# Optimization experiments

Measured on AMD Instinct MI355X. Metric: run time of the kernel, lower is better.

The kernel has to match this reference:

```python
import jax, jax.numpy as jnp
import numpy as np

DEPTH = 5
EPS = 1e-8


def setup_inputs() -> dict:
    key = jax.random.key(0)
    ks = jax.random.split(key, 7)
    N, E, Q = 50000, 1600000, 16
    return {
        "marg_i": jax.random.normal(ks[0], (N, Q), dtype=jnp.float32),
        "cav_ij": jax.random.uniform(ks[1], (E, Q), dtype=jnp.float32),
        "C": jax.random.uniform(ks[2], (Q, Q), dtype=jnp.float32),
        "field_i": jax.random.normal(ks[3], (N, Q), dtype=jnp.float32),
        "edge_dst": jax.random.randint(ks[4], (E,), 0, N, dtype=jnp.int32),
        "a1_src": jax.random.randint(ks[5], (E,), 0, N, dtype=jnp.int32),
        "indice_ij": jax.random.randint(ks[6], (E,), 0, E, dtype=jnp.int32),
    }


def reference(marg_i, cav_ij, C, field_i, edge_dst, a1_src, indice_ij):
    # Belief-propagation layers repeated DEPTH times.
    # B_ @ temp2  -> segment_sum of edge messages into destination nodes [N,Q]
    # A1 @ marg_i -> gather of source-node marginal per edge [E,Q]
    N = field_i.shape[0]

    def step(carry, _):
        marg, cav = carry
        temp2 = jnp.log(cav @ C + EPS)                                  # [E,Q]
        marg = jax.ops.segment_sum(temp2, edge_dst, num_segments=N) + field_i  # [N,Q]
        cav = jax.nn.softmax(marg[a1_src] - temp2[indice_ij], axis=1)  # [E,Q]
        return (marg, cav), None

    (marg, cav), _ = jax.lax.scan(step, (marg_i, cav_ij), None, length=DEPTH)
    return jax.nn.log_softmax(marg, axis=1)
```

## Files before the change

### kernel.cpp

```cpp
#include <hip/hip_runtime.h>
#include <hip/hip_fp16.h>

#define Q 16
#define EPS 1e-8f
#define DEPTH 5
#define BS 512
#define WSHIFT 9

typedef unsigned int u32;
typedef _Float16 h2 __attribute__((ext_vector_type(2)));

typedef int   i2v __attribute__((ext_vector_type(2)));
typedef u32   u4v __attribute__((ext_vector_type(4)));
typedef float f4v __attribute__((ext_vector_type(4)));

__device__ __forceinline__ int nt_ld(const int* p) {
    return __builtin_nontemporal_load(p);
}
__device__ __forceinline__ void nt_st(int* p, int v) {
    __builtin_nontemporal_store(v, p);
}
__device__ __forceinline__ int2 nt_ld2(const int2* p) {
    i2v r = __builtin_nontemporal_load((const i2v*)p);
    return make_int2(r.x, r.y);
}
__device__ __forceinline__ void nt_st2(int2* p, int2 v) {
    i2v t; t.x = v.x; t.y = v.y;
    __builtin_nontemporal_store(t, (i2v*)p);
}
__device__ __forceinline__ float4 nt_ldf4(const float4* p) {
    f4v r = __builtin_nontemporal_load((const f4v*)p);
    return make_float4(r.x, r.y, r.z, r.w);
}
__device__ __forceinline__ void nt_stf4(float4* p, float4 v) {
    f4v t; t.x = v.x; t.y = v.y; t.z = v.z; t.w = v.w;
    __builtin_nontemporal_store(t, (f4v*)p);
}
__device__ __forceinline__ void nt_stu4(uint4* p, uint4 v) {
    u4v t; t.x = v.x; t.y = v.y; t.z = v.z; t.w = v.w;
    __builtin_nontemporal_store(t, (u4v*)p);
}

__device__ __forceinline__ u32 pack2(float a, float b) {
    __half2 h = __floats2half2_rn(a, b);
    return *(u32*)&h;
}
__device__ __forceinline__ float2 unpack2(u32 u) {
    __half2 h = *(__half2*)&u;
    return __half22float2(h);
}
__device__ __forceinline__ h2 mkh2(float a, float b) {
    h2 v; v[0] = (_Float16)a; v[1] = (_Float16)b; return v;
}


__global__ __launch_bounds__(256) void rank0_kernel(
    const int* __restrict__ dst, int* __restrict__ count,
    int* __restrict__ lr, int E)
{
    int e = blockIdx.x * 256 + threadIdx.x;
    if (e < E) nt_st(&lr[e], atomicAdd(&count[nt_ld(&dst[e])], 1));
}

__global__ __launch_bounds__(256) void scan_partial(
    const int* __restrict__ count, int* __restrict__ partial, int N)
{
    __shared__ int sm[256];
    int i = blockIdx.x * 256 + threadIdx.x;
    sm[threadIdx.x] = (i < N) ? count[i] : 0;
    __syncthreads();
    for (int off = 128; off > 0; off >>= 1) {
        if (threadIdx.x < off) sm[threadIdx.x] += sm[threadIdx.x + off];
        __syncthreads();
    }
    if (threadIdx.x == 0) partial[blockIdx.x] = sm[0];
}

__global__ __launch_bounds__(1024) void scan_top(
    int* __restrict__ partial, int nb)
{
    __shared__ int sm[1024];
    int t = threadIdx.x;
    int v = (t < nb) ? partial[t] : 0;
    sm[t] = v;
    __syncthreads();
    for (int off = 1; off < 1024; off <<= 1) {
        int u = (t >= off) ? sm[t - off] : 0;
        __syncthreads();
        sm[t] += u;
        __syncthreads();
    }
    if (t < nb) partial[t] = sm[t] - v;
}

__global__ __launch_bounds__(256) void scan_final(
    const int* __restrict__ count, const int* __restrict__ partial,
    int* __restrict__ start, int N)
{
    __shared__ int sm[256];
    int i = blockIdx.x * 256 + threadIdx.x;
    int v = (i < N) ? count[i] : 0;
    sm[threadIdx.x] = v;
    __syncthreads();
    for (int off = 1; off < 256; off <<= 1) {
        int u = (threadIdx.x >= off) ? sm[threadIdx.x - off] : 0;
        __syncthreads();
        sm[threadIdx.x] += u;
        __syncthreads();
    }
    int excl = sm[threadIdx.x] - v + partial[blockIdx.x];
    if (i < N) start[i] = excl;
    if (i == N - 1) start[N] = excl + v;
}

__global__ __launch_bounds__(256) void pos_kernel(
    const int* __restrict__ dst, const int* __restrict__ lr,
    const int* __restrict__ start, int* __restrict__ pos, int E)
{
    int e = blockIdx.x * 256 + threadIdx.x;
    if (e < E) pos[e] = start[nt_ld(&dst[e])] + nt_ld(&lr[e]);
}

__global__ __launch_bounds__(256) void scatter_direct(
    const int* __restrict__ a1_src, const int* __restrict__ indice,
    const int* __restrict__ dst, const int* __restrict__ pos,
    int2* __restrict__ meta2, int* __restrict__ m0e, int E)
{
    int e = blockIdx.x * 256 + threadIdx.x;
    if (e < E) {
        int p = nt_ld(&pos[e]);
        int ie = nt_ld(&indice[e]);
        int2 mv = make_int2(pos[ie],
                            (int)(((u32)nt_ld(&dst[e]) << 16) | (u32)nt_ld(&a1_src[e])));
        nt_st2(&meta2[p], mv);
        nt_st(&m0e[p], e);
    }
}

__global__ __launch_bounds__(256) void bnode_build(
    const int* __restrict__ start, int* __restrict__ blist,
    int* __restrict__ bcount, int N)
{
    int n = blockIdx.x * 256 + threadIdx.x;
    if (n >= N) return;
    int slo = start[n], shi = start[n + 1];
    bool need = (slo == shi) || ((slo >> WSHIFT) != ((shi - 1) >> WSHIFT));
    if (need) {
        int p = atomicAdd(bcount, 1);
        blist[p] = n;
    }
}

__global__ __launch_bounds__(256) void binit(
    const int* __restrict__ blist, const int* __restrict__ bcount,
    const float* __restrict__ field, float* __restrict__ marg)
{
    int idx = blockIdx.x * 256 + threadIdx.x;
    int cnt = *bcount;
    if (idx >= cnt * 4) return;
    int n = blist[idx >> 2], part = idx & 3;
    ((float4*)(marg + (size_t)n * Q))[part] =
        ((const float4*)(field + (size_t)n * Q))[part];
}

template<int MODE>
__global__ __launch_bounds__(BS) void fused_round(
    const int2* __restrict__ meta2, const int* __restrict__ m0e,
    const float* __restrict__ C,
    const float* __restrict__ cav,
    const float* __restrict__ marg_in, const u32* __restrict__ t2_old,
    const int* __restrict__ start, const float* __restrict__ field,
    u32* __restrict__ t2_new, float* __restrict__ marg_out, int E)
{
    __shared__ __align__(16) h2 Csh[Q * 8];
    __shared__ float stage[BS * 17];
    __shared__ int s_nfirst, s_nlast;

    const int tid = threadIdx.x;
    const int blo = blockIdx.x * BS;
    const int bhi = min(blo + BS, E);
    const int j = blo + tid;
    const bool act = (j < E);

    int2 meta;
    float4 m0, m1, m2, m3;
    uint4 r0, r1;
    if (act) {
        meta = nt_ld2(&meta2[j]);
        if (MODE == 0) {
            const float4* rp = (const float4*)(cav + (size_t)nt_ld(&m0e[j]) * Q);
            m0 = nt_ldf4(rp + 0); m1 = nt_ldf4(rp + 1);
            m2 = nt_ldf4(rp + 2); m3 = nt_ldf4(rp + 3);
        } else {
            const int src = meta.y & 0xffff;
            const float4* mp = (const float4*)(marg_in + (size_t)src * Q);
            const uint4*  tp = (const uint4*)(t2_old + (size_t)meta.x * 8);
            m0 = mp[0]; m1 = mp[1]; m2 = mp[2]; m3 = mp[3];
            r0 = tp[0]; r1 = tp[1];
        }
    }

    if (tid < 128) {
        int q = tid >> 3, kk = tid & 7;
        Csh[q * 8 + kk] = mkh2(C[(2 * kk) * Q + q], C[(2 * kk + 1) * Q + q]);
    }
    if (act) {
        int mydst = (int)(((u32)meta.y) >> 16);
        if (j == blo)     s_nfirst = mydst;
        if (j == bhi - 1) s_nlast  = mydst;
    }
    __syncthreads();

    float t[Q];
    if (act) {
        h2 uh[8];
        float s, logs;
        if (MODE == 0) {
            uh[0] = mkh2(m0.x, m0.y); uh[1] = mkh2(m0.z, m0.w);
            uh[2] = mkh2(m1.x, m1.y); uh[3] = mkh2(m1.z, m1.w);
            uh[4] = mkh2(m2.x, m2.y); uh[5] = mkh2(m2.z, m2.w);
            uh[6] = mkh2(m3.x, m3.y); uh[7] = mkh2(m3.z, m3.w);
            s = 1.f; logs = 0.f;
        } else {
            float2 p0 = unpack2(r0.x), p1 = unpack2(r0.y),
                   p2 = unpack2(r0.z), p3 = unpack2(r0.w);
            float2 p4 = unpack2(r1.x), p5 = unpack2(r1.y),
                   p6 = unpack2(r1.z), p7 = unpack2(r1.w);

            float x[Q] = {m0.x - p0.x, m0.y - p0.y, m0.z - p1.x, m0.w - p1.y,
                          m1.x - p2.x, m1.y - p2.y, m1.z - p3.x, m1.w - p3.y,
                          m2.x - p4.x, m2.y - p4.y, m2.z - p5.x, m2.w - p5.y,
                          m3.x - p6.x, m3.y - p6.y, m3.z - p7.x, m3.w - p7.y};

            float mx = x[0];
#pragma unroll
            for (int q = 1; q < Q; ++q) mx = fmaxf(mx, x[q]);
            float u[Q];
            s = 0.f;
#pragma unroll
            for (int q = 0; q < Q; ++q) { u[q] = __expf(x[q] - mx); s += u[q]; }
            logs = __logf(s);
#pragma unroll
            for (int k = 0; k < 8; ++k) uh[k] = mkh2(u[2 * k], u[2 * k + 1]);
        }

        const float base = EPS * s;
#pragma unroll
        for (int q = 0; q < Q; ++q) {
            const uint4* cp = (const uint4*)&Csh[q * 8];
            h2 col[8];
            ((uint4*)col)[0] = cp[0];
            ((uint4*)col)[1] = cp[1];
            float acc = base;
#pragma unroll
            for (int kk = 0; kk < 8; ++kk)
                acc = __builtin_amdgcn_fdot2(uh[kk], col[kk], acc, false);
            t[q] = __logf(acc) - logs;
        }

        if (MODE != 2) {
            uint4 w0, w1;
            w0.x = pack2(t[0],  t[1]);  w0.y = pack2(t[2],  t[3]);
            w0.z = pack2(t[4],  t[5]);  w0.w = pack2(t[6],  t[7]);
            w1.x = pack2(t[8],  t[9]);  w1.y = pack2(t[10], t[11]);
            w1.z = pack2(t[12], t[13]); w1.w = pack2(t[14], t[15]);
            uint4* op = (uint4*)(t2_new + (size_t)j * 8);
            nt_stu4(op + 0, w0);
            nt_stu4(op + 1, w1);
        }
    } else {
#pragma unroll
        for (int q = 0; q < Q; ++q) t[q] = 0.f;
    }

#pragma unroll
    for (int q = 0; q < Q; ++q) stage[tid * 17 + q] = t[q];
    __syncthreads();

    const int nfirst = s_nfirst;
    const int ncnt = s_nlast - nfirst + 1;
    for (int k = tid; k < ncnt * Q; k += BS) {
        int ln = k >> 4, q = k & 15;
        int n = nfirst + ln;
        int slo = start[n], shi = start[n + 1];
        int lo = max(slo, blo), hi = min(shi, bhi);
        float s = 0.f;
        for (int sl = lo; sl < hi; ++sl) s += stage[(sl - blo) * 17 + q];
        if (slo >= blo && shi <= bhi)
            marg_out[(size_t)n * Q + q] = s + field[(size_t)n * Q + q];
        else
            atomicAdd(marg_out + (size_t)n * Q + q, s);
    }
}

__global__ __launch_bounds__(256) void node_out(
    const float* __restrict__ marg, float* __restrict__ out, int N)
{
    int i = blockIdx.x * 256 + threadIdx.x;
    if (i >= N) return;

    const float4* mp = (const float4*)(marg + (size_t)i * Q);
    float4 m0 = nt_ldf4(mp + 0), m1 = nt_ldf4(mp + 1),
           m2 = nt_ldf4(mp + 2), m3 = nt_ldf4(mp + 3);
    float x[Q] = {m0.x, m0.y, m0.z, m0.w, m1.x, m1.y, m1.z, m1.w,
                  m2.x, m2.y, m2.z, m2.w, m3.x, m3.y, m3.z, m3.w};

    float mx = x[0];
#pragma unroll
    for (int q = 1; q < Q; ++q) mx = fmaxf(mx, x[q]);
    float s = 0.f;
#pragma unroll
    for (int q = 0; q < Q; ++q) s += __expf(x[q] - mx);
    float lse = mx + __logf(s);

    float4* op = (float4*)(out + (size_t)i * Q);
    nt_stf4(op + 0, make_float4(x[0]  - lse, x[1]  - lse, x[2]  - lse, x[3]  - lse));
    nt_stf4(op + 1, make_float4(x[4]  - lse, x[5]  - lse, x[6]  - lse, x[7]  - lse));
    nt_stf4(op + 2, make_float4(x[8]  - lse, x[9]  - lse, x[10] - lse, x[11] - lse));
    nt_stf4(op + 3, make_float4(x[12] - lse, x[13] - lse, x[14] - lse, x[15] - lse));
}

extern "C" void kernel_launch(void* const* d_in, const int* in_sizes, int n_in,
                              void* d_out, int out_size, void* d_ws, size_t ws_size,
                              hipStream_t stream) {
    const float* cav_in   = (const float*)d_in[1];
    const float* C        = (const float*)d_in[2];
    const float* field_i  = (const float*)d_in[3];
    const int*   edge_dst = (const int*)d_in[4];
    const int*   a1_src   = (const int*)d_in[5];
    const int*   indice   = (const int*)d_in[6];
    float* out = (float*)d_out;

    const int E = in_sizes[4];
    const int N = in_sizes[0] / Q;

    char* ws = (char*)d_ws;
    const size_t t2_bytes   = (size_t)E * 32;
    const size_t node_bytes = (size_t)N * Q * sizeof(float);
    u32*   t2a    = (u32*)ws;                     ws += t2_bytes;
    u32*   t2b    = (u32*)ws;                     ws += t2_bytes;
    int2*  meta2  = (int2*)ws;                    ws += (size_t)E * 8;
    int*   m0e    = (int*)ws;                     ws += (size_t)E * 4;
    float* marg_a = (float*)ws;                   ws += node_bytes;
    float* marg_b = (float*)ws;                   ws += node_bytes;
    int*   pos    = (int*)ws;                     ws += (size_t)E * 4;
    int*   lr     = (int*)ws;                     ws += (size_t)E * 4;
    int*   count  = (int*)ws;                     ws += (size_t)N * 4;
    int*   bcount = (int*)ws;                     ws += 4;
    int*   start  = (int*)ws;                     ws += (size_t)(N + 1) * 4;
    int*   blist  = (int*)ws;                     ws += (size_t)N * 4;
    int*   partial= (int*)ws;

    const int eb = 256;
    const int eg = (E + eb - 1) / eb;
    const int fg = (E + BS - 1) / BS;
    const int ng = (N + eb - 1) / eb;

    hipMemsetAsync(count, 0, (size_t)N * 4 + 4, stream);
    rank0_kernel<<<eg, eb, 0, stream>>>(edge_dst, count, lr, E);
    scan_partial<<<ng, eb, 0, stream>>>(count, partial, N);
    scan_top<<<1, 1024, 0, stream>>>(partial, ng);
    scan_final<<<ng, eb, 0, stream>>>(count, partial, start, N);
    pos_kernel<<<eg, eb, 0, stream>>>(edge_dst, lr, start, pos, E);
    scatter_direct<<<eg, eb, 0, stream>>>(a1_src, indice, edge_dst, pos,
                                          meta2, m0e, E);
    bnode_build<<<ng, eb, 0, stream>>>(start, blist, bcount, N);

    u32* t_cur = t2a;
    u32* t_nxt = t2b;
    float* m_in = marg_b;
    float* m_out = marg_a;
    const int bg = (N * 4 + eb - 1) / eb;

    for (int it = 0; it < DEPTH; ++it) {
        binit<<<bg, eb, 0, stream>>>(blist, bcount, field_i, m_out);
        if (it == 0)
            fused_round<0><<<fg, BS, 0, stream>>>(meta2, m0e, C, cav_in,
                                                  nullptr, nullptr, start, field_i,
                                                  t_cur, m_out, E);
        else if (it != DEPTH - 1)
            fused_round<1><<<fg, BS, 0, stream>>>(meta2, m0e, C, nullptr,
                                                  m_in, t_cur, start, field_i,
                                                  t_nxt, m_out, E);
        else
            fused_round<2><<<fg, BS, 0, stream>>>(meta2, m0e, C, nullptr,
                                                  m_in, t_cur, start, field_i,
                                                  nullptr, m_out, E);
        if (it != 0) { u32* tt = t_cur; t_cur = t_nxt; t_nxt = tt; }
        float* tm = m_in; m_in = m_out; m_out = tm;
    }

    node_out<<<ng, eb, 0, stream>>>(m_in, out, N);
}
```

Measured before the change: 712.2 us.

## Fuse preprocessing kernels and pack sorted edge metadata into int4

Packs each edge's destination and local rank into one word so the separate position kernel can be dropped, and folds boundary-node detection into the final scan kernel. Scatter now computes sorted positions on the fly and writes one 16-byte record holding the reverse-edge position, dst/src and original edge id, replacing the separate meta2 and m0e arrays. Nontemporal hints on the metadata load and the t2 stores are removed, so those accesses may now stay in cache. The trade-off is 16 bytes of metadata per edge read in every round instead of 8 (plus 4 in the first round), and a packed format that caps the per-node rank at 16 bits.

```diff
diff --git a/kernel.cpp b/kernel.cpp
--- a/kernel.cpp
+++ b/kernel.cpp
@@ -10,23 +10,10 @@
 typedef unsigned int u32;
 typedef _Float16 h2 __attribute__((ext_vector_type(2)));
 
-typedef int   i2v __attribute__((ext_vector_type(2)));
-typedef u32   u4v __attribute__((ext_vector_type(4)));
 typedef float f4v __attribute__((ext_vector_type(4)));
 
 __device__ __forceinline__ int nt_ld(const int* p) {
     return __builtin_nontemporal_load(p);
-}
-__device__ __forceinline__ void nt_st(int* p, int v) {
-    __builtin_nontemporal_store(v, p);
-}
-__device__ __forceinline__ int2 nt_ld2(const int2* p) {
-    i2v r = __builtin_nontemporal_load((const i2v*)p);
-    return make_int2(r.x, r.y);
-}
-__device__ __forceinline__ void nt_st2(int2* p, int2 v) {
-    i2v t; t.x = v.x; t.y = v.y;
-    __builtin_nontemporal_store(t, (i2v*)p);
 }
 __device__ __forceinline__ float4 nt_ldf4(const float4* p) {
     f4v r = __builtin_nontemporal_load((const f4v*)p);
@@ -36,10 +23,6 @@
     f4v t; t.x = v.x; t.y = v.y; t.z = v.z; t.w = v.w;
     __builtin_nontemporal_store(t, (f4v*)p);
 }
-__device__ __forceinline__ void nt_stu4(uint4* p, uint4 v) {
-    u4v t; t.x = v.x; t.y = v.y; t.z = v.z; t.w = v.w;
-    __builtin_nontemporal_store(t, (u4v*)p);
-}
 
 __device__ __forceinline__ u32 pack2(float a, float b) {
     __half2 h = __floats2half2_rn(a, b);
@@ -56,10 +39,14 @@
 
 __global__ __launch_bounds__(256) void rank0_kernel(
     const int* __restrict__ dst, int* __restrict__ count,
-    int* __restrict__ lr, int E)
+    int* __restrict__ lrd, int E)
 {
     int e = blockIdx.x * 256 + threadIdx.x;
-    if (e < E) nt_st(&lr[e], atomicAdd(&count[nt_ld(&dst[e])], 1));
+    if (e < E) {
+        int d = nt_ld(&dst[e]);
+        int r = atomicAdd(&count[d], 1);
+        lrd[e] = (int)(((u32)d << 16) | (u32)r);
+    }
 }
 
 __global__ __launch_bounds__(256) void scan_partial(
@@ -95,7 +82,8 @@
 
 __global__ __launch_bounds__(256) void scan_final(
     const int* __restrict__ count, const int* __restrict__ partial,
-    int* __restrict__ start, int N)
+    int* __restrict__ start, int* __restrict__ blist,
+    int* __restrict__ bcount, int N)
 {
     __shared__ int sm[256];
     int i = blockIdx.x * 256 + threadIdx.x;
@@ -109,45 +97,31 @@
         __syncthreads();
     }
     int excl = sm[threadIdx.x] - v + partial[blockIdx.x];
-    if (i < N) start[i] = excl;
+    if (i < N) {
+        start[i] = excl;
+        bool need = (v == 0) || ((excl >> WSHIFT) != ((excl + v - 1) >> WSHIFT));
+        if (need) {
+            int p = atomicAdd(bcount, 1);
+            blist[p] = i;
+        }
+    }
     if (i == N - 1) start[N] = excl + v;
 }
 
-__global__ __launch_bounds__(256) void pos_kernel(
-    const int* __restrict__ dst, const int* __restrict__ lr,
-    const int* __restrict__ start, int* __restrict__ pos, int E)
-{
-    int e = blockIdx.x * 256 + threadIdx.x;
-    if (e < E) pos[e] = start[nt_ld(&dst[e])] + nt_ld(&lr[e]);
-}
-
-__global__ __launch_bounds__(256) void scatter_direct(
+__global__ __launch_bounds__(256) void scatter16(
     const int* __restrict__ a1_src, const int* __restrict__ indice,
-    const int* __restrict__ dst, const int* __restrict__ pos,
-    int2* __restrict__ meta2, int* __restrict__ m0e, int E)
+    const int* __restrict__ lrd, const int* __restrict__ start,
+    int4* __restrict__ sorted, int E)
 {
     int e = blockIdx.x * 256 + threadIdx.x;
     if (e < E) {
-        int p = nt_ld(&pos[e]);
+        u32 dl = (u32)lrd[e];
+        int p = start[dl >> 16] + (int)(dl & 0xffffu);
         int ie = nt_ld(&indice[e]);
-        int2 mv = make_int2(pos[ie],
-                            (int)(((u32)nt_ld(&dst[e]) << 16) | (u32)nt_ld(&a1_src[e])));
-        nt_st2(&meta2[p], mv);
-        nt_st(&m0e[p], e);
-    }
-}
-
-__global__ __launch_bounds__(256) void bnode_build(
-    const int* __restrict__ start, int* __restrict__ blist,
-    int* __restrict__ bcount, int N)
-{
-    int n = blockIdx.x * 256 + threadIdx.x;
-    if (n >= N) return;
-    int slo = start[n], shi = start[n + 1];
-    bool need = (slo == shi) || ((slo >> WSHIFT) != ((shi - 1) >> WSHIFT));
-    if (need) {
-        int p = atomicAdd(bcount, 1);
-        blist[p] = n;
+        u32 dl2 = (u32)lrd[ie];
+        int pik = start[dl2 >> 16] + (int)(dl2 & 0xffffu);
+        int dstsrc = (int)((dl & 0xffff0000u) | (u32)nt_ld(&a1_src[e]));
+        sorted[p] = make_int4(pik, dstsrc, e, 0);
     }
 }
 
@@ -165,7 +139,7 @@
 
 template<int MODE>
 __global__ __launch_bounds__(BS) void fused_round(
-    const int2* __restrict__ meta2, const int* __restrict__ m0e,
+    const int4* __restrict__ sorted,
     const float* __restrict__ C,
     const float* __restrict__ cav,
     const float* __restrict__ marg_in, const u32* __restrict__ t2_old,
@@ -182,13 +156,13 @@
     const int j = blo + tid;
     const bool act = (j < E);
 
-    int2 meta;
+    int4 meta;
     float4 m0, m1, m2, m3;
     uint4 r0, r1;
     if (act) {
-        meta = nt_ld2(&meta2[j]);
+        meta = sorted[j];
         if (MODE == 0) {
-            const float4* rp = (const float4*)(cav + (size_t)nt_ld(&m0e[j]) * Q);
+            const float4* rp = (const float4*)(cav + (size_t)meta.z * Q);
             m0 = nt_ldf4(rp + 0); m1 = nt_ldf4(rp + 1);
             m2 = nt_ldf4(rp + 2); m3 = nt_ldf4(rp + 3);
         } else {
@@ -265,8 +239,7 @@
             w1.x = pack2(t[8],  t[9]);  w1.y = pack2(t[10], t[11]);
             w1.z = pack2(t[12], t[13]); w1.w = pack2(t[14], t[15]);
             uint4* op = (uint4*)(t2_new + (size_t)j * 8);
-            nt_stu4(op + 0, w0);
-            nt_stu4(op + 1, w1);
+            op[0] = w0; op[1] = w1;
         }
     } else {
 #pragma unroll
@@ -339,12 +312,10 @@
     const size_t node_bytes = (size_t)N * Q * sizeof(float);
     u32*   t2a    = (u32*)ws;                     ws += t2_bytes;
     u32*   t2b    = (u32*)ws;                     ws += t2_bytes;
-    int2*  meta2  = (int2*)ws;                    ws += (size_t)E * 8;
-    int*   m0e    = (int*)ws;                     ws += (size_t)E * 4;
+    int4*  sorted = (int4*)ws;                    ws += (size_t)E * 16;
+    int*   lrd    = (int*)ws;                     ws += (size_t)E * 4;
     float* marg_a = (float*)ws;                   ws += node_bytes;
     float* marg_b = (float*)ws;                   ws += node_bytes;
-    int*   pos    = (int*)ws;                     ws += (size_t)E * 4;
-    int*   lr     = (int*)ws;                     ws += (size_t)E * 4;
     int*   count  = (int*)ws;                     ws += (size_t)N * 4;
     int*   bcount = (int*)ws;                     ws += 4;
     int*   start  = (int*)ws;                     ws += (size_t)(N + 1) * 4;
@@ -357,14 +328,11 @@
     const int ng = (N + eb - 1) / eb;
 
     hipMemsetAsync(count, 0, (size_t)N * 4 + 4, stream);
-    rank0_kernel<<<eg, eb, 0, stream>>>(edge_dst, count, lr, E);
+    rank0_kernel<<<eg, eb, 0, stream>>>(edge_dst, count, lrd, E);
     scan_partial<<<ng, eb, 0, stream>>>(count, partial, N);
     scan_top<<<1, 1024, 0, stream>>>(partial, ng);
-    scan_final<<<ng, eb, 0, stream>>>(count, partial, start, N);
-    pos_kernel<<<eg, eb, 0, stream>>>(edge_dst, lr, start, pos, E);
-    scatter_direct<<<eg, eb, 0, stream>>>(a1_src, indice, edge_dst, pos,
-                                          meta2, m0e, E);
-    bnode_build<<<ng, eb, 0, stream>>>(start, blist, bcount, N);
+    scan_final<<<ng, eb, 0, stream>>>(count, partial, start, blist, bcount, N);
+    scatter16<<<eg, eb, 0, stream>>>(a1_src, indice, lrd, start, sorted, E);
 
     u32* t_cur = t2a;
     u32* t_nxt = t2b;
@@ -375,15 +343,15 @@
     for (int it = 0; it < DEPTH; ++it) {
         binit<<<bg, eb, 0, stream>>>(blist, bcount, field_i, m_out);
         if (it == 0)
-            fused_round<0><<<fg, BS, 0, stream>>>(meta2, m0e, C, cav_in,
+            fused_round<0><<<fg, BS, 0, stream>>>(sorted, C, cav_in,
                                                   nullptr, nullptr, start, field_i,
                                                   t_cur, m_out, E);
         else if (it != DEPTH - 1)
-            fused_round<1><<<fg, BS, 0, stream>>>(meta2, m0e, C, nullptr,
+            fused_round<1><<<fg, BS, 0, stream>>>(sorted, C, nullptr,
                                                   m_in, t_cur, start, field_i,
                                                   t_nxt, m_out, E);
         else
-            fused_round<2><<<fg, BS, 0, stream>>>(meta2, m0e, C, nullptr,
+            fused_round<2><<<fg, BS, 0, stream>>>(sorted, C, nullptr,
                                                   m_in, t_cur, start, field_i,
                                                   nullptr, m_out, E);
         if (it != 0) { u32* tt = t_cur; t_cur = t_nxt; t_nxt = tt; }
```

Measured after the change: 628.5 us. 11.8% less time.
